# Performance work log

Measured on AMD Instinct MI355X. Metric: run time of the kernel, lower is better.

## Reference

```python
import math
import jax, jax.numpy as jnp
import numpy as np

B, T, D = 512, 512, 256
ALPHA = 0.5
BETA = 0.9


def setup_inputs() -> dict:
    key = jax.random.key(0)
    ks = jax.random.split(key, 9)
    s = 1.0 / math.sqrt(D)
    return {
        "window_features": jax.random.normal(ks[0], (B, T, D), jnp.float32),
        "timestamps": jax.random.uniform(ks[1], (B, T), jnp.float32) * 86400.0 * 7,
        "prev_L": jax.random.normal(ks[2], (B, D), jnp.float32),
        "prev_M": jax.random.uniform(ks[3], (B, 1), jnp.float32),
        "pad_mask": jnp.zeros((B, T), jnp.bool_),
        "W_Q": jax.random.normal(ks[4], (D, D), jnp.float32) * s,
        "W_K": jax.random.normal(ks[5], (D, D), jnp.float32) * s,
        "W_V": jax.random.normal(ks[6], (D, D), jnp.float32) * s,
        "cls_w": jax.random.normal(ks[7], (1, 2 * D + 1), jnp.float32) * s,
        "cls_b": jnp.zeros((1,), jnp.float32),
    }


def reference(window_features, timestamps, prev_L, prev_M, pad_mask,
              W_Q, W_K, W_V, cls_w, cls_b):
    Bv, Tv, d = window_features.shape
    valid = ~pad_mask
    valid_f = valid.astype(window_features.dtype)              # [B,T]
    valid_count = jnp.clip(valid_f.sum(1, keepdims=True), 1.0)  # [B,1]

    # decay weights from recency (days)
    t_masked = jnp.where(pad_mask, -1e18, timestamps)
    t_max = t_masked.max(1, keepdims=True)                      # [B,1]
    dt = jnp.clip(t_max - timestamps, 0.0) / 86400.0
    lam = jnp.exp(-ALPHA * dt) * valid_f                        # [B,T]

    # mean-pooled query
    q = (window_features * valid_f[..., None]).sum(1) / valid_count  # [B,d]
    Q = q @ W_Q.T                                               # [B,d]
    K = jnp.einsum('btd,ed->bte', window_features, W_K)         # [B,T,d]
    V = jnp.einsum('btd,ed->bte', window_features, W_V)         # [B,T,d]

    scores = jnp.einsum('bd,btd->bt', Q, K) / math.sqrt(d)      # [B,T]
    scores = jnp.where(pad_mask, -1e9, scores)
    attn = jax.nn.softmax(scores, axis=-1)

    # decay-modulated reweighting + renormalization
    w = lam * attn
    w = w / (w.sum(1, keepdims=True) + 1e-8)

    L_t = jnp.einsum('bt,btd->bd', w, V)                        # [B,d]
    delta_t = L_t - prev_L
    M_t = BETA * prev_M + (1.0 - BETA) * jnp.linalg.norm(delta_t, axis=1, keepdims=True)
    T_event = jnp.concatenate([L_t, delta_t, M_t], axis=-1)     # [B,2d+1]
    p = (T_event @ cls_w.T + cls_b).squeeze(-1)                 # [B]
    return (p, T_event, L_t, M_t)
```

## Files before the change

### kernel.cpp

```cpp
#include <hip/hip_runtime.h>
#include <math.h>

#define ALPHA 0.5f
#define BETA 0.9f
#define Bsz 512
#define Tsz 512
#define Dsz 256

__device__ __forceinline__ float wave_reduce_sum(float v) {
    v += __shfl_xor(v, 32, 64);
    v += __shfl_xor(v, 16, 64);
    v += __shfl_xor(v, 8, 64);
    v += __shfl_xor(v, 4, 64);
    v += __shfl_xor(v, 2, 64);
    v += __shfl_xor(v, 1, 64);
    return v;
}

__device__ __forceinline__ float wave_reduce_max(float v) {
    v = fmaxf(v, __shfl_xor(v, 32, 64));
    v = fmaxf(v, __shfl_xor(v, 16, 64));
    v = fmaxf(v, __shfl_xor(v, 8, 64));
    v = fmaxf(v, __shfl_xor(v, 4, 64));
    v = fmaxf(v, __shfl_xor(v, 2, 64));
    v = fmaxf(v, __shfl_xor(v, 1, 64));
    return v;
}

__global__ __launch_bounds__(512, 4) void fused(const float* __restrict__ x,
                                                const float* __restrict__ ts,
                                                const unsigned char* __restrict__ pad,
                                                const float* __restrict__ WQ,
                                                const float* __restrict__ WK,
                                                const float* __restrict__ WV,
                                                const float* __restrict__ prevL,
                                                const float* __restrict__ prevM,
                                                const float* __restrict__ clsw,
                                                const float* __restrict__ clsb,
                                                float* __restrict__ out) {
    const int b = blockIdx.x;
    const int tid = threadIdx.x;
    const int w = tid >> 6, lane = tid & 63;
    const int rloc = lane >> 3;
    const int sub = lane & 7;

    __shared__ float lamS[Tsz];
    __shared__ float okS[Tsz];
    __shared__ float part[8][Dsz];
    __shared__ float qS[Dsz];
    __shared__ float QS[Dsz];
    __shared__ __align__(16) float qkS[Dsz];
    __shared__ float xwS[Dsz];
    __shared__ float EGS[16];
    __shared__ float red[16];
    __shared__ float red2[8];
    __shared__ float tmaxS, cntS;

    {
        bool v = (pad[(size_t)b * Tsz + tid] == 0);
        float tv = ts[(size_t)b * Tsz + tid];
        okS[tid] = v ? 1.f : 0.f;
        lamS[tid] = tv;
        float lmax = v ? tv : -1e30f;
        float lcnt = v ? 1.f : 0.f;
        lmax = wave_reduce_max(lmax);
        lcnt = wave_reduce_sum(lcnt);
        if (lane == 0) { red[w] = lmax; red[8 + w] = lcnt; }
    }
    __syncthreads();
    if (tid == 0) {
        float m = -1e30f, c = 0.f;
        #pragma unroll
        for (int i = 0; i < 8; ++i) { m = fmaxf(m, red[i]); c += red[8 + i]; }
        tmaxS = m;
        cntS = fmaxf(c, 1.f);
    }
    __syncthreads();
    {
        float dt = fmaxf(tmaxS - lamS[tid], 0.f) * (1.f / 86400.f);
        lamS[tid] = okS[tid] * __expf(-ALPHA * dt);
    }

    const float* xb = x + (size_t)b * Tsz * Dsz;
    {
        float4 a0 = make_float4(0.f, 0.f, 0.f, 0.f);
        float4 a1 = a0, a2 = a0, a3 = a0;
        const int tbase = w * 64;
        for (int i = 0; i < 64; i += 4) {
            const int t = tbase + i;
            float4 x0 = *(const float4*)(xb + (size_t)(t + 0) * Dsz + lane * 4);
            float4 x1 = *(const float4*)(xb + (size_t)(t + 1) * Dsz + lane * 4);
            float4 x2 = *(const float4*)(xb + (size_t)(t + 2) * Dsz + lane * 4);
            float4 x3 = *(const float4*)(xb + (size_t)(t + 3) * Dsz + lane * 4);
            const float v0 = okS[t], v1 = okS[t + 1], v2 = okS[t + 2], v3 = okS[t + 3];
            a0.x += v0 * x0.x; a0.y += v0 * x0.y; a0.z += v0 * x0.z; a0.w += v0 * x0.w;
            a1.x += v1 * x1.x; a1.y += v1 * x1.y; a1.z += v1 * x1.z; a1.w += v1 * x1.w;
            a2.x += v2 * x2.x; a2.y += v2 * x2.y; a2.z += v2 * x2.z; a2.w += v2 * x2.w;
            a3.x += v3 * x3.x; a3.y += v3 * x3.y; a3.z += v3 * x3.z; a3.w += v3 * x3.w;
        }
        part[w][lane * 4 + 0] = (a0.x + a1.x) + (a2.x + a3.x);
        part[w][lane * 4 + 1] = (a0.y + a1.y) + (a2.y + a3.y);
        part[w][lane * 4 + 2] = (a0.z + a1.z) + (a2.z + a3.z);
        part[w][lane * 4 + 3] = (a0.w + a1.w) + (a2.w + a3.w);
    }
    __syncthreads();
    if (tid < Dsz) {
        float s = 0.f;
        #pragma unroll
        for (int w2 = 0; w2 < 8; ++w2) s += part[w2][tid];
        qS[tid] = s / cntS;
    }
    __syncthreads();

    {
        const int i = tid & 255, half = tid >> 8;
        const float* wq = WQ + (size_t)i * Dsz + half * 128;
        const float* qh = qS + half * 128;
        float acc = 0.f;
        #pragma unroll 4
        for (int d4 = 0; d4 < 128; d4 += 4) {
            float4 wv = *(const float4*)(wq + d4);
            acc += wv.x * qh[d4] + wv.y * qh[d4 + 1] + wv.z * qh[d4 + 2] + wv.w * qh[d4 + 3];
        }
        part[half][i] = acc;
    }
    __syncthreads();
    if (tid < Dsz) QS[tid] = part[0][tid] + part[1][tid];
    __syncthreads();

    {
        const int d = tid & 255, half = tid >> 8;
        const int e0 = half * 128;
        float v0 = 0.f, v1 = 0.f, v2 = 0.f, v3 = 0.f;
        #pragma unroll 4
        for (int e = e0; e < e0 + 128; e += 4) {
            v0 += QS[e + 0] * WK[(size_t)(e + 0) * Dsz + d];
            v1 += QS[e + 1] * WK[(size_t)(e + 1) * Dsz + d];
            v2 += QS[e + 2] * WK[(size_t)(e + 2) * Dsz + d];
            v3 += QS[e + 3] * WK[(size_t)(e + 3) * Dsz + d];
        }
        part[half][d] = (v0 + v1) + (v2 + v3);
    }
    __syncthreads();
    if (tid < Dsz) qkS[tid] = (part[0][tid] + part[1][tid]) * 0.0625f;
    __syncthreads();

    float4 qkr[8];
    #pragma unroll
    for (int jj = 0; jj < 8; ++jj)
        qkr[jj] = *(const float4*)(&qkS[(jj * 8 + sub) << 2]);

    float4 acc = make_float4(0.f, 0.f, 0.f, 0.f);
    float E = 0.f, G = 0.f;
    {
        const int rowbase = w * 64;
        for (int gi = 7; gi >= 0; --gi) {
            const int base = rowbase + gi * 8;
            const int r = base + rloc;
            const float* rp = xb + (size_t)r * Dsz;
            float s = 0.f;
            #pragma unroll
            for (int jj = 0; jj < 8; ++jj) {
                const float4 xv = *(const float4*)(rp + ((jj * 8 + sub) << 2));
                s += xv.x * qkr[jj].x + xv.y * qkr[jj].y + xv.z * qkr[jj].z + xv.w * qkr[jj].w;
            }
            s += __shfl_xor(s, 1, 64);
            s += __shfl_xor(s, 2, 64);
            s += __shfl_xor(s, 4, 64);
            const float e = okS[r] * __expf(s);
            const float g = lamS[r] * e;
            E += e; G += g;
            #pragma unroll
            for (int k = 0; k < 8; ++k) {
                const float gk = __shfl(g, k * 8, 64);
                const float4 xa = *(const float4*)(xb + (size_t)(base + k) * Dsz + lane * 4);
                acc.x += gk * xa.x; acc.y += gk * xa.y; acc.z += gk * xa.z; acc.w += gk * xa.w;
            }
        }
    }
    part[w][lane * 4 + 0] = acc.x;
    part[w][lane * 4 + 1] = acc.y;
    part[w][lane * 4 + 2] = acc.z;
    part[w][lane * 4 + 3] = acc.w;
    {
        float Ew = wave_reduce_sum(E) * 0.125f;
        float Gw = wave_reduce_sum(G) * 0.125f;
        if (lane == 0) { EGS[w] = Ew; EGS[8 + w] = Gw; }
    }
    __syncthreads();
    if (tid < Dsz) {
        float Et = 0.f, Gt = 0.f;
        #pragma unroll
        for (int i = 0; i < 8; ++i) { Et += EGS[i]; Gt += EGS[8 + i]; }
        float denom = Gt + 1e-8f * Et;
        float accd = 0.f;
        #pragma unroll
        for (int w2 = 0; w2 < 8; ++w2) accd += part[w2][tid];
        xwS[tid] = (denom > 0.f) ? accd / denom : 0.f;
    }
    __syncthreads();

    {
        const int i = tid & 255, half = tid >> 8;
        const float* wv = WV + (size_t)i * Dsz + half * 128;
        const float* xh = xwS + half * 128;
        float a = 0.f;
        #pragma unroll 4
        for (int d4 = 0; d4 < 128; d4 += 4) {
            float4 wvv = *(const float4*)(wv + d4);
            a += wvv.x * xh[d4] + wvv.y * xh[d4 + 1] + wvv.z * xh[d4 + 2] + wvv.w * xh[d4 + 3];
        }
        part[half][i] = a;
    }
    __syncthreads();

    float Le = 0.f, delta = 0.f, pp = 0.f;
    if (tid < Dsz) {
        Le = part[0][tid] + part[1][tid];
        delta = Le - prevL[(size_t)b * Dsz + tid];
        pp = Le * clsw[tid] + delta * clsw[Dsz + tid];
    }
    float ssq = wave_reduce_sum(delta * delta);
    float psum = wave_reduce_sum(pp);
    if (lane == 0) { red[w] = ssq; red2[w] = psum; }
    __syncthreads();

    if (tid < Dsz) {
        float sr = 0.f;
        #pragma unroll
        for (int i = 0; i < 8; ++i) sr += red[i];
        float nrm = sqrtf(sr);
        float M = BETA * prevM[b] + (1.f - BETA) * nrm;

        float* out_p = out;
        float* out_T = out + Bsz;
        float* out_L = out + Bsz + (size_t)Bsz * (2 * Dsz + 1);
        float* out_M = out + Bsz + (size_t)Bsz * (2 * Dsz + 1) + (size_t)Bsz * Dsz;

        out_T[(size_t)b * (2 * Dsz + 1) + tid] = Le;
        out_T[(size_t)b * (2 * Dsz + 1) + Dsz + tid] = delta;
        out_L[(size_t)b * Dsz + tid] = Le;
        if (tid == 0) {
            float ps = 0.f;
            #pragma unroll
            for (int i = 0; i < 8; ++i) ps += red2[i];
            float p = ps + M * clsw[2 * Dsz] + clsb[0];
            out_p[b] = p;
            out_T[(size_t)b * (2 * Dsz + 1) + 2 * Dsz] = M;
            out_M[b] = M;
        }
    }
}

extern "C" void kernel_launch(void* const* d_in, const int* in_sizes, int n_in,
                              void* d_out, int out_size, void* d_ws, size_t ws_size,
                              hipStream_t stream) {
    const float* x     = (const float*)d_in[0];
    const float* ts    = (const float*)d_in[1];
    const float* prevL = (const float*)d_in[2];
    const float* prevM = (const float*)d_in[3];
    const unsigned char* pad = (const unsigned char*)d_in[4];
    const float* WQ    = (const float*)d_in[5];
    const float* WK    = (const float*)d_in[6];
    const float* WV    = (const float*)d_in[7];
    const float* clsw  = (const float*)d_in[8];
    const float* clsb  = (const float*)d_in[9];

    (void)d_ws; (void)ws_size;

    fused<<<Bsz, 512, 0, stream>>>(x, ts, pad, WQ, WK, WV, prevL, prevM, clsw, clsb,
                                   (float*)d_out);
}
```

Before: 464.0 us.

## Reuse score-pass row loads for weighted value accumulation, reduce across lanes

```diff
diff --git a/kernel.cpp b/kernel.cpp
--- a/kernel.cpp
+++ b/kernel.cpp
@@ -46,7 +46,7 @@
 
     __shared__ float lamS[Tsz];
     __shared__ float okS[Tsz];
-    __shared__ float part[8][Dsz];
+    __shared__ __align__(16) float part[8][Dsz];
     __shared__ float qS[Dsz];
     __shared__ float QS[Dsz];
     __shared__ __align__(16) float qkS[Dsz];
@@ -150,38 +150,75 @@
     for (int jj = 0; jj < 8; ++jj)
         qkr[jj] = *(const float4*)(&qkS[(jj * 8 + sub) << 2]);
 
-    float4 acc = make_float4(0.f, 0.f, 0.f, 0.f);
+    float4 acc0 = make_float4(0.f, 0.f, 0.f, 0.f);
+    float4 acc1 = acc0, acc2 = acc0, acc3 = acc0, acc4 = acc0, acc5 = acc0, acc6 = acc0, acc7 = acc0;
     float E = 0.f, G = 0.f;
     {
         const int rowbase = w * 64;
         for (int gi = 7; gi >= 0; --gi) {
-            const int base = rowbase + gi * 8;
-            const int r = base + rloc;
+            const int r = rowbase + gi * 8 + rloc;
             const float* rp = xb + (size_t)r * Dsz;
-            float s = 0.f;
-            #pragma unroll
-            for (int jj = 0; jj < 8; ++jj) {
-                const float4 xv = *(const float4*)(rp + ((jj * 8 + sub) << 2));
-                s += xv.x * qkr[jj].x + xv.y * qkr[jj].y + xv.z * qkr[jj].z + xv.w * qkr[jj].w;
-            }
+            float4 xv0 = *(const float4*)(rp + ((0 * 8 + sub) << 2));
+            float4 xv1 = *(const float4*)(rp + ((1 * 8 + sub) << 2));
+            float4 xv2 = *(const float4*)(rp + ((2 * 8 + sub) << 2));
+            float4 xv3 = *(const float4*)(rp + ((3 * 8 + sub) << 2));
+            float4 xv4 = *(const float4*)(rp + ((4 * 8 + sub) << 2));
+            float4 xv5 = *(const float4*)(rp + ((5 * 8 + sub) << 2));
+            float4 xv6 = *(const float4*)(rp + ((6 * 8 + sub) << 2));
+            float4 xv7 = *(const float4*)(rp + ((7 * 8 + sub) << 2));
+            float s = xv0.x * qkr[0].x + xv0.y * qkr[0].y + xv0.z * qkr[0].z + xv0.w * qkr[0].w
+                    + xv1.x * qkr[1].x + xv1.y * qkr[1].y + xv1.z * qkr[1].z + xv1.w * qkr[1].w
+                    + xv2.x * qkr[2].x + xv2.y * qkr[2].y + xv2.z * qkr[2].z + xv2.w * qkr[2].w
+                    + xv3.x * qkr[3].x + xv3.y * qkr[3].y + xv3.z * qkr[3].z + xv3.w * qkr[3].w
+                    + xv4.x * qkr[4].x + xv4.y * qkr[4].y + xv4.z * qkr[4].z + xv4.w * qkr[4].w
+                    + xv5.x * qkr[5].x + xv5.y * qkr[5].y + xv5.z * qkr[5].z + xv5.w * qkr[5].w
+                    + xv6.x * qkr[6].x + xv6.y * qkr[6].y + xv6.z * qkr[6].z + xv6.w * qkr[6].w
+                    + xv7.x * qkr[7].x + xv7.y * qkr[7].y + xv7.z * qkr[7].z + xv7.w * qkr[7].w;
             s += __shfl_xor(s, 1, 64);
             s += __shfl_xor(s, 2, 64);
             s += __shfl_xor(s, 4, 64);
             const float e = okS[r] * __expf(s);
             const float g = lamS[r] * e;
             E += e; G += g;
-            #pragma unroll
-            for (int k = 0; k < 8; ++k) {
-                const float gk = __shfl(g, k * 8, 64);
-                const float4 xa = *(const float4*)(xb + (size_t)(base + k) * Dsz + lane * 4);
-                acc.x += gk * xa.x; acc.y += gk * xa.y; acc.z += gk * xa.z; acc.w += gk * xa.w;
-            }
-        }
-    }
-    part[w][lane * 4 + 0] = acc.x;
-    part[w][lane * 4 + 1] = acc.y;
-    part[w][lane * 4 + 2] = acc.z;
-    part[w][lane * 4 + 3] = acc.w;
+            acc0.x += g * xv0.x; acc0.y += g * xv0.y; acc0.z += g * xv0.z; acc0.w += g * xv0.w;
+            acc1.x += g * xv1.x; acc1.y += g * xv1.y; acc1.z += g * xv1.z; acc1.w += g * xv1.w;
+            acc2.x += g * xv2.x; acc2.y += g * xv2.y; acc2.z += g * xv2.z; acc2.w += g * xv2.w;
+            acc3.x += g * xv3.x; acc3.y += g * xv3.y; acc3.z += g * xv3.z; acc3.w += g * xv3.w;
+            acc4.x += g * xv4.x; acc4.y += g * xv4.y; acc4.z += g * xv4.z; acc4.w += g * xv4.w;
+            acc5.x += g * xv5.x; acc5.y += g * xv5.y; acc5.z += g * xv5.z; acc5.w += g * xv5.w;
+            acc6.x += g * xv6.x; acc6.y += g * xv6.y; acc6.z += g * xv6.z; acc6.w += g * xv6.w;
+            acc7.x += g * xv7.x; acc7.y += g * xv7.y; acc7.z += g * xv7.z; acc7.w += g * xv7.w;
+        }
+    }
+    #pragma unroll
+    for (int step = 8; step <= 32; step <<= 1) {
+        acc0.x += __shfl_xor(acc0.x, step, 64); acc0.y += __shfl_xor(acc0.y, step, 64);
+        acc0.z += __shfl_xor(acc0.z, step, 64); acc0.w += __shfl_xor(acc0.w, step, 64);
+        acc1.x += __shfl_xor(acc1.x, step, 64); acc1.y += __shfl_xor(acc1.y, step, 64);
+        acc1.z += __shfl_xor(acc1.z, step, 64); acc1.w += __shfl_xor(acc1.w, step, 64);
+        acc2.x += __shfl_xor(acc2.x, step, 64); acc2.y += __shfl_xor(acc2.y, step, 64);
+        acc2.z += __shfl_xor(acc2.z, step, 64); acc2.w += __shfl_xor(acc2.w, step, 64);
+        acc3.x += __shfl_xor(acc3.x, step, 64); acc3.y += __shfl_xor(acc3.y, step, 64);
+        acc3.z += __shfl_xor(acc3.z, step, 64); acc3.w += __shfl_xor(acc3.w, step, 64);
+        acc4.x += __shfl_xor(acc4.x, step, 64); acc4.y += __shfl_xor(acc4.y, step, 64);
+        acc4.z += __shfl_xor(acc4.z, step, 64); acc4.w += __shfl_xor(acc4.w, step, 64);
+        acc5.x += __shfl_xor(acc5.x, step, 64); acc5.y += __shfl_xor(acc5.y, step, 64);
+        acc5.z += __shfl_xor(acc5.z, step, 64); acc5.w += __shfl_xor(acc5.w, step, 64);
+        acc6.x += __shfl_xor(acc6.x, step, 64); acc6.y += __shfl_xor(acc6.y, step, 64);
+        acc6.z += __shfl_xor(acc6.z, step, 64); acc6.w += __shfl_xor(acc6.w, step, 64);
+        acc7.x += __shfl_xor(acc7.x, step, 64); acc7.y += __shfl_xor(acc7.y, step, 64);
+        acc7.z += __shfl_xor(acc7.z, step, 64); acc7.w += __shfl_xor(acc7.w, step, 64);
+    }
+    if (rloc == 0) {
+        *(float4*)&part[w][(0 * 8 + sub) << 2] = acc0;
+        *(float4*)&part[w][(1 * 8 + sub) << 2] = acc1;
+        *(float4*)&part[w][(2 * 8 + sub) << 2] = acc2;
+        *(float4*)&part[w][(3 * 8 + sub) << 2] = acc3;
+        *(float4*)&part[w][(4 * 8 + sub) << 2] = acc4;
+        *(float4*)&part[w][(5 * 8 + sub) << 2] = acc5;
+        *(float4*)&part[w][(6 * 8 + sub) << 2] = acc6;
+        *(float4*)&part[w][(7 * 8 + sub) << 2] = acc7;
+    }
     {
         float Ew = wave_reduce_sum(E) * 0.125f;
         float Gw = wave_reduce_sum(G) * 0.125f;
```

Result: slower. 505.5 us (+9.0%).
